# Optimization experiments

Hardware: AMD Instinct MI355X
Metric: run time of the kernel (lower is better)

The kernel has to match this reference:

```python
import jax, jax.numpy as jnp
import numpy as np
import math

RADIUS2 = 0.1 * 0.1   # QueryAndGroup(0.1, 64)
NSAMPLE = 64
NEG_SLOPE = 0.2


def get_lattice_points(b, n):
    # AtlasNet-style regular UV grid in [0,1]^2, first n points of a ceil(sqrt(n))^2 grid
    side = int(math.ceil(math.sqrt(n)))
    u = jnp.linspace(0.0, 1.0, side, dtype=jnp.float32)
    gx, gy = jnp.meshgrid(u, u, indexing='ij')
    pts = jnp.stack([gx.ravel(), gy.ravel()], axis=-1)[:n]  # (n, 2)
    return jnp.broadcast_to(pts[None], (b, n, 2))


def conv1x1(x, W, b):
    # 1x1 Conv1d == per-point GEMM: x (B,Cin,N), W (Cout,Cin), b (Cout,)
    return jnp.einsum('oc,bcn->bon', W, x) + b[None, :, None]


def mlp(x, params):
    for W, b in params:
        x = jax.nn.leaky_relu(conv1x1(x, W, b), NEG_SLOPE)
    return x


def ball_group_max(points, feats):
    # points (B,N,3), feats (B,C,N). Ball query (radius 0.1, first 64 in index
    # order, pad with first hit) + feature gather + max over neighborhood.
    B, N, _ = points.shape
    sq = jnp.sum(points * points, axis=-1)  # (B,N)
    d2 = sq[:, :, None] + sq[:, None, :] - 2.0 * jnp.einsum('bnd,bmd->bnm', points, points)
    mask = d2 < RADIUS2                                    # (B,N,N)
    cand = jnp.where(mask, jnp.arange(N, dtype=jnp.int32)[None, None, :], N)
    idx = jnp.sort(cand, axis=-1)[:, :, :NSAMPLE]          # first NSAMPLE hits
    first = idx[:, :, :1]
    idx = jnp.where(idx == N, first, idx)                  # pad with first hit (self always hits)
    idx = jnp.minimum(idx, N - 1)
    ft = jnp.swapaxes(feats, 1, 2)                         # (B,N,C)
    gathered = ft[jnp.arange(B)[:, None, None], idx]       # (B,N,K,C)
    return jnp.swapaxes(gathered.max(axis=2), 1, 2)        # (B,C,N)


def setup_inputs() -> dict:
    key = jax.random.key(0)
    ks = jax.random.split(key, 20)
    s = 0.05
    inp = {
        'z':   jax.random.normal(ks[0], (2, 512), dtype=jnp.float32),
        'W1a': jax.random.normal(ks[1], (512, 514), dtype=jnp.float32) * s,
        'b1a': jnp.zeros((512,), jnp.float32),
        'W1b': jax.random.normal(ks[2], (512, 512), dtype=jnp.float32) * s,
        'b1b': jnp.zeros((512,), jnp.float32),
        'W1c': jax.random.normal(ks[3], (512, 512), dtype=jnp.float32) * s,
        'b1c': jnp.zeros((512,), jnp.float32),
        'Wx1': jax.random.normal(ks[4], (3, 512), dtype=jnp.float32) * s,
        'bx1': jnp.zeros((3,), jnp.float32),
        'W2a': jax.random.normal(ks[5], (512, 1536), dtype=jnp.float32) * s,
        'b2a': jnp.zeros((512,), jnp.float32),
        'W2b': jax.random.normal(ks[6], (512, 512), dtype=jnp.float32) * s,
        'b2b': jnp.zeros((512,), jnp.float32),
        'W2c': jax.random.normal(ks[7], (512, 512), dtype=jnp.float32) * s,
        'b2c': jnp.zeros((512,), jnp.float32),
        'Wx2': jax.random.normal(ks[8], (3, 512), dtype=jnp.float32) * s,
        'bx2': jnp.zeros((3,), jnp.float32),
        'n1': 1024,
        'n2': 2048,
    }
    return inp


def reference(z, W1a, b1a, W1b, b1b, W1c, b1c, Wx1, bx1,
              W2a, b2a, W2b, b2b, W2c, b2c, Wx2, bx2, n1, n2):
    B, dim = z.shape

    def stage1(n):
        latt = get_lattice_points(B, n)                                    # (B,n,2)
        zc = jnp.concatenate([jnp.broadcast_to(z[:, None, :], (B, n, dim)), latt], axis=2)
        x = jnp.swapaxes(zc, 1, 2)                                         # (B,514,n)
        h = mlp(x, [(W1a, b1a), (W1b, b1b), (W1c, b1c)])                   # (B,512,n)
        pts = jnp.swapaxes(jax.nn.sigmoid(conv1x1(h, Wx1, bx1)), 1, 2) - 0.5
        return h, pts

    _, first_stage_points = stage1(n1)
    h2, fine_points = stage1(n2)

    local = ball_group_max(fine_points, h2)                                # (B,512,n2)
    glob = jnp.broadcast_to(h2.max(axis=2, keepdims=True), h2.shape)       # (B,512,n2)
    feat = jnp.concatenate([h2, local, glob], axis=1)                      # (B,1536,n2)

    f = mlp(feat, [(W2a, b2a), (W2b, b2b), (W2c, b2c)])
    delta = 0.1 * (jax.nn.sigmoid(conv1x1(f, Wx2, bx2)) - 0.5)
    second_stage_points = jnp.swapaxes(delta, 1, 2) + fine_points
    return (first_stage_points, second_stage_points, fine_points)
```

## Files before the change

kernel.cpp:

```cpp
#include <hip/hip_runtime.h>
#include <math.h>

#define B 2
#define N1 1024
#define N2 2048
#define R1TOT 6144
#define R2TOT 4096
#define SLOPE 0.2f

typedef short bf16x8 __attribute__((ext_vector_type(8)));
typedef float f32x4 __attribute__((ext_vector_type(4)));
typedef unsigned short u16x4 __attribute__((ext_vector_type(4)));
typedef unsigned short u16x8 __attribute__((ext_vector_type(8)));

__device__ __forceinline__ unsigned short f2bf(float x) {
    unsigned int u = __float_as_uint(x);
    unsigned int r = (u + 0x7fffu + ((u >> 16) & 1u)) >> 16;
    return (unsigned short)r;
}
__device__ __forceinline__ float bf2f(unsigned short h) {
    return __uint_as_float(((unsigned int)h) << 16);
}
__device__ __forceinline__ unsigned fenc(float f) {
    unsigned u = __float_as_uint(f);
    return (u & 0x80000000u) ? ~u : (u | 0x80000000u);
}
__device__ __forceinline__ float fdec(unsigned u) {
    unsigned b = (u & 0x80000000u) ? (u & 0x7FFFFFFFu) : ~u;
    return __uint_as_float(b);
}

#define OFF_WP     0
#define OFF_X1P    6291456
#define OFF_XMP    18874368
#define OFF_X2P    31457280
#define OFF_X3P    39845888
#define OFF_X4P    44040192
#define OFF_C1     48234496
#define OFF_GLOBE  48238592
#define OFF_GBIAS  48242688
#define OFF_HACC1  48246784
#define OFF_HACC2  48345088
#define ZERO_WORDS 43008

__global__ void k_prep(const float* __restrict__ W1b, const float* __restrict__ W1c,
                       const float* __restrict__ W2b, const float* __restrict__ W2c,
                       const float* __restrict__ W2a, unsigned short* __restrict__ wp,
                       const float* __restrict__ z, const float* __restrict__ W1a,
                       const float* __restrict__ b1a, float* __restrict__ c1,
                       float* __restrict__ zbase) {
    int bx = blockIdx.x, tid = threadIdx.x;
    if (bx < 6144) {
        int idx = bx * 256 + tid;
        const float* src; unsigned short* dst; int o, k, K, in_ld;
        if (idx < 1048576) {
            int which = idx >> 18; int local = idx & 262143;
            K = 512; in_ld = 512;
            src = (which == 0) ? W1b : (which == 1) ? W1c : (which == 2) ? W2b : W2c;
            dst = wp + (long)which * 524288;
            o = local >> 9; k = local & 511;
        } else {
            int local = idx - 1048576;
            K = 1024; in_ld = 1536; src = W2a; dst = wp + 2097152;
            o = local >> 10; k = local & 1023;
        }
        float v = src[(long)o * in_ld + k];
        unsigned short hi = f2bf(v);
        dst[(long)o * 2 * K + k] = hi;
        dst[(long)o * 2 * K + K + k] = f2bf(v - bf2f(hi));
    } else if (bx < 6152) {
        for (int l = (bx - 6144) * 256 + tid; l < ZERO_WORDS; l += 2048) zbase[l] = 0.f;
    } else {
        int gid = (bx - 6152) * 4 + (tid >> 6);
        int lane = tid & 63;
        int b = gid >> 9, o = gid & 511;
        float acc = 0.f;
        const float* wr = W1a + (long)o * 514;
        const float* zb = z + b * 512;
        for (int k = lane; k < 512; k += 64) acc += wr[k] * zb[k];
        #pragma unroll
        for (int off = 32; off > 0; off >>= 1) acc += __shfl_down(acc, off, 64);
        if (lane == 0) c1[gid] = acc + b1a[o];
    }
}

__global__ void k_layer_a(const float* __restrict__ W1a, const float* __restrict__ c1,
                          unsigned short* __restrict__ X1) {
    int idx = blockIdx.x * 256 + threadIdx.x;
    int o = idx & 511;
    int r = idx >> 9;
    int b, n, side;
    if (r < 2048) { b = r >> 10; n = r & 1023; side = 32; }
    else          { int r2 = r - 2048; b = r2 >> 11; n = r2 & 2047; side = 46; }
    int row = n / side, col = n % side;
    double inv = 1.0 / (double)(side - 1);
    float lx = (row == side - 1) ? 1.0f : (float)(row * inv);
    float ly = (col == side - 1) ? 1.0f : (float)(col * inv);
    float h = c1[b * 512 + o] + W1a[(long)o * 514 + 512] * lx + W1a[(long)o * 514 + 513] * ly;
    h = (h > 0.f) ? h : SLOPE * h;
    unsigned short hi = f2bf(h);
    X1[(long)r * 1024 + o] = hi;
    X1[(long)r * 1024 + 512 + o] = f2bf(h - bf2f(hi));
}

template<int TERMS>
__global__ __launch_bounds__(256, 2) void k_gemm(
    const unsigned short* __restrict__ Wp, int ldw,
    const unsigned short* __restrict__ Xp, int ldx,
    int K,
    const float* __restrict__ bias, int bias_div,
    unsigned short* __restrict__ Xn, int ldxn, int lo_off, int row_off, int pack_min,
    const float* __restrict__ Wx, float* __restrict__ hacc,
    unsigned* __restrict__ globE, int glob_min) {

    __shared__ __align__(16) char sm[32768];
    const int t = threadIdx.x;
    const int nb0 = blockIdx.x * 64;
    const int ob0 = blockIdx.y * 64;

    const unsigned short* gp[8];
    int lo_[8];
    #pragma unroll
    for (int p = 0; p < 8; ++p) {
        const int T = p >> 1;
        if (TERMS == 1 && (T == 1 || T == 3)) continue;
        int j2 = ((p & 1) << 8) + t;
        int r = j2 >> 3, cl = j2 & 7, cs = cl ^ (r & 7);
        gp[p] = (T < 2)
            ? (Wp + (long)(ob0 + r) * ldw + ((T == 1) ? K : 0) + cs * 8)
            : (Xp + (long)(nb0 + r) * ldx + ((T == 3) ? K : 0) + cs * 8);
        lo_[p] = p * 4096 + t * 16;
    }

    const int lane = t & 63, w = t >> 6;
    const int wy = w >> 1, wx = w & 1;
    const int quad = lane >> 4, l15 = lane & 15;
    const int xm = l15 & 7;
    const int rowA = (wy * 32 + l15) * 128;
    const int rowB = (wx * 32 + l15) * 128;
    const int ca0 = (quad ^ xm) * 16;
    const int ca1 = ((quad + 4) ^ xm) * 16;

    f32x4 acc[2][2];
    #pragma unroll
    for (int i = 0; i < 2; ++i)
        #pragma unroll
        for (int j = 0; j < 2; ++j) { f32x4 zz = {0.f, 0.f, 0.f, 0.f}; acc[i][j] = zz; }

    for (int k0 = 0; k0 < K; k0 += 64) {
        #pragma unroll
        for (int p = 0; p < 8; ++p) {
            const int T = p >> 1;
            if (TERMS == 1 && (T == 1 || T == 3)) continue;
            __builtin_amdgcn_global_load_lds(
                (const __attribute__((address_space(1))) void*)(const void*)(gp[p] + k0),
                (__attribute__((address_space(3))) void*)(void*)(sm + lo_[p]),
                16, 0, 0);
        }
        __syncthreads();
        #pragma unroll
        for (int sub = 0; sub < 2; ++sub) {
            const int cb = (sub == 0) ? ca0 : ca1;
            bf16x8 ah[2], bh[2];
            #pragma unroll
            for (int i = 0; i < 2; ++i)
                ah[i] = *(const bf16x8*)(const void*)(sm + rowA + i * 2048 + cb);
            #pragma unroll
            for (int j = 0; j < 2; ++j)
                bh[j] = *(const bf16x8*)(const void*)(sm + 16384 + rowB + j * 2048 + cb);
            if (TERMS == 3) {
                bf16x8 al[2], bl[2];
                #pragma unroll
                for (int i = 0; i < 2; ++i)
                    al[i] = *(const bf16x8*)(const void*)(sm + 8192 + rowA + i * 2048 + cb);
                #pragma unroll
                for (int j = 0; j < 2; ++j)
                    bl[j] = *(const bf16x8*)(const void*)(sm + 24576 + rowB + j * 2048 + cb);
                #pragma unroll
                for (int i = 0; i < 2; ++i)
                    #pragma unroll
                    for (int j = 0; j < 2; ++j) {
                        acc[i][j] = __builtin_amdgcn_mfma_f32_16x16x32_bf16(ah[i], bh[j], acc[i][j], 0, 0, 0);
                        acc[i][j] = __builtin_amdgcn_mfma_f32_16x16x32_bf16(ah[i], bl[j], acc[i][j], 0, 0, 0);
                        acc[i][j] = __builtin_amdgcn_mfma_f32_16x16x32_bf16(al[i], bh[j], acc[i][j], 0, 0, 0);
                    }
            } else {
                #pragma unroll
                for (int i = 0; i < 2; ++i)
                    #pragma unroll
                    for (int j = 0; j < 2; ++j)
                        acc[i][j] = __builtin_amdgcn_mfma_f32_16x16x32_bf16(ah[i], bh[j], acc[i][j], 0, 0, 0);
            }
        }
        __syncthreads();
    }

    float val[2][2][4];
    #pragma unroll
    for (int j = 0; j < 2; ++j) {
        int n = nb0 + wx * 32 + j * 16 + l15;
        int bidx0 = (bias_div >= (1 << 29)) ? 0 : (n / bias_div) * 512;
        #pragma unroll
        for (int i = 0; i < 2; ++i) {
            int ob = ob0 + wy * 32 + i * 16 + quad * 4;
            #pragma unroll
            for (int r = 0; r < 4; ++r) {
                float x = acc[i][j][r] + bias[bidx0 + ob + r];
                val[i][j][r] = (x > 0.f) ? x : SLOPE * x;
            }
        }
        if (Xn && n >= pack_min) {
            long nl = n - row_off;
            #pragma unroll
            for (int i = 0; i < 2; ++i) {
                int ob = ob0 + wy * 32 + i * 16 + quad * 4;
                u16x4 h4;
                #pragma unroll
                for (int r = 0; r < 4; ++r) h4[r] = f2bf(val[i][j][r]);
                *(u16x4*)(void*)(Xn + nl * ldxn + ob) = h4;
                if (lo_off) {
                    u16x4 l4;
                    #pragma unroll
                    for (int r = 0; r < 4; ++r) l4[r] = f2bf(val[i][j][r] - bf2f(h4[r]));
                    *(u16x4*)(void*)(Xn + nl * ldxn + lo_off + ob) = l4;
                }
            }
        }
    }

    if (hacc) {
        __syncthreads();
        float* smh = (float*)sm;
        unsigned* smg = (unsigned*)(sm + 1024);
        if (t < 256) smh[t] = 0.f;
        if (t < 64) smg[t] = 0u;
        __syncthreads();
        float wxv[3][2][4];
        #pragma unroll
        for (int ch = 0; ch < 3; ++ch)
            #pragma unroll
            for (int i = 0; i < 2; ++i)
                #pragma unroll
                for (int r = 0; r < 4; ++r)
                    wxv[ch][i][r] = Wx[ch * 512 + ob0 + wy * 32 + i * 16 + quad * 4 + r];
        #pragma unroll
        for (int j = 0; j < 2; ++j) {
            int nl = wx * 32 + j * 16 + l15;
            float p0 = 0.f, p1 = 0.f, p2 = 0.f;
            #pragma unroll
            for (int i = 0; i < 2; ++i)
                #pragma unroll
                for (int r = 0; r < 4; ++r) {
                    float v = val[i][j][r];
                    p0 += v * wxv[0][i][r];
                    p1 += v * wxv[1][i][r];
                    p2 += v * wxv[2][i][r];
                }
            atomicAdd(&smh[nl * 4 + 0], p0);
            atomicAdd(&smh[nl * 4 + 1], p1);
            atomicAdd(&smh[nl * 4 + 2], p2);
        }
        if (globE && nb0 >= glob_min) {
            #pragma unroll
            for (int i = 0; i < 2; ++i)
                #pragma unroll
                for (int r = 0; r < 4; ++r) {
                    float mx = fmaxf(val[i][0][r], val[i][1][r]);
                    atomicMax(&smg[wy * 32 + i * 16 + quad * 4 + r], fenc(mx));
                }
        }
        __syncthreads();
        if (t < 64) {
            atomicAdd(&hacc[(long)(nb0 + t) * 4 + 0], smh[t * 4 + 0]);
            atomicAdd(&hacc[(long)(nb0 + t) * 4 + 1], smh[t * 4 + 1]);
            atomicAdd(&hacc[(long)(nb0 + t) * 4 + 2], smh[t * 4 + 2]);
            if (globE && nb0 >= glob_min) {
                int b = (nb0 - glob_min) >> 11;
                atomicMax(&globE[b * 512 + ob0 + t], smg[t]);
            }
        }
    }
}

__global__ void k_finalize(const float* __restrict__ bx1, const float* __restrict__ hacc1,
                           float* __restrict__ out0, float* __restrict__ out2,
                           const float* __restrict__ W2a, const float* __restrict__ b2a,
                           const unsigned* __restrict__ globE, float* __restrict__ gbias) {
    int bx = blockIdx.x, tid = threadIdx.x;
    if (bx < 24) {
        int r = bx * 256 + tid;
        float* dst = (r < 2048) ? (out0 + (long)r * 3) : (out2 + (long)(r - 2048) * 3);
        #pragma unroll
        for (int ch = 0; ch < 3; ++ch) {
            float a = hacc1[(long)r * 4 + ch] + bx1[ch];
            dst[ch] = 1.f / (1.f + expf(-a)) - 0.5f;
        }
    } else {
        int gid = (bx - 24) * 4 + (tid >> 6);
        int lane = tid & 63;
        int b = gid >> 9, o = gid & 511;
        float acc = 0.f;
        const float* wr = W2a + (long)o * 1536 + 1024;
        for (int k = lane; k < 512; k += 64) acc += wr[k] * fdec(globE[b * 512 + k]);
        #pragma unroll
        for (int off = 32; off > 0; off >>= 1) acc += __shfl_down(acc, off, 64);
        if (lane == 0) gbias[gid] = acc + b2a[o];
    }
}

__global__ __launch_bounds__(256) void k_ball(const float* __restrict__ fine,
                                              unsigned short* __restrict__ X2P) {
    int i = blockIdx.x, b = blockIdx.y;
    int tid = threadIdx.x, lane = tid & 63, wv = tid >> 6;
    __shared__ int idxl[64];
    __shared__ int wcnt[4];
    __shared__ float part[8][256];
    const float* fb = fine + (long)b * N2 * 3;
    float xi = fb[i * 3 + 0], yi = fb[i * 3 + 1], zi = fb[i * 3 + 2];
    float sqi = __fadd_rn(__fadd_rn(__fmul_rn(xi, xi), __fmul_rn(yi, yi)), __fmul_rn(zi, zi));
    int cnt = 0;
    for (int it = 0; it < N2 / 256; ++it) {
        int j = it * 256 + tid;
        float xj = fb[j * 3 + 0], yj = fb[j * 3 + 1], zj = fb[j * 3 + 2];
        float sqj = __fadd_rn(__fadd_rn(__fmul_rn(xj, xj), __fmul_rn(yj, yj)), __fmul_rn(zj, zj));
        float dot = __fadd_rn(__fadd_rn(__fmul_rn(xi, xj), __fmul_rn(yi, yj)), __fmul_rn(zi, zj));
        float d2 = __fsub_rn(__fadd_rn(sqi, sqj), __fmul_rn(2.0f, dot));
        bool pred = d2 < 0.01f;
        unsigned long long m = __ballot(pred);
        if (lane == 0) wcnt[wv] = __popcll(m);
        __syncthreads();
        int wbase = cnt;
        #pragma unroll
        for (int q = 0; q < 3; ++q) { if (q < wv) wbase += wcnt[q]; }
        int total = wcnt[0] + wcnt[1] + wcnt[2] + wcnt[3];
        int rank = wbase + __popcll(m & ((1ull << lane) - 1ull));
        if (pred && rank < 64) idxl[rank] = j;
        cnt += total;
        if (cnt >= 64) break;
        __syncthreads();
    }
    __syncthreads();
    int m = min(cnt, 64);

    const unsigned short* hb = X2P + (long)b * N2 * 1024;
    int g = tid & 63, q = tid >> 6;
    float mx[8];
    #pragma unroll
    for (int r = 0; r < 8; ++r) mx[r] = -1e30f;
    for (int jj = q; jj < m; jj += 4) {
        u16x8 v = *(const u16x8*)(const void*)(hb + (long)idxl[jj] * 1024 + g * 8);
        #pragma unroll
        for (int r = 0; r < 8; ++r) mx[r] = fmaxf(mx[r], bf2f(v[r]));
    }
    #pragma unroll
    for (int r = 0; r < 8; ++r) part[r][tid] = mx[r];
    __syncthreads();
    if (tid < 64) {
        unsigned short* orow = X2P + (long)(b * N2 + i) * 1024;
        u16x8 hi;
        #pragma unroll
        for (int r = 0; r < 8; ++r) {
            float v0 = fmaxf(fmaxf(part[r][tid], part[r][tid + 64]),
                             fmaxf(part[r][tid + 128], part[r][tid + 192]));
            hi[r] = (unsigned short)(__float_as_uint(v0) >> 16);
        }
        *(u16x8*)(void*)(orow + 512 + tid * 8) = hi;
    }
}

__global__ void k_final2(const float* __restrict__ bx2, const float* __restrict__ hacc2,
                         const float* __restrict__ fine, float* __restrict__ out1) {
    int r = blockIdx.x * 256 + threadIdx.x;
    #pragma unroll
    for (int ch = 0; ch < 3; ++ch) {
        float a = hacc2[(long)r * 4 + ch] + bx2[ch];
        out1[(long)r * 3 + ch] = fine[(long)r * 3 + ch] + 0.1f * (1.f / (1.f + expf(-a)) - 0.5f);
    }
}

extern "C" void kernel_launch(void* const* d_in, const int* in_sizes, int n_in,
                              void* d_out, int out_size, void* d_ws, size_t ws_size,
                              hipStream_t stream) {
    const float* z   = (const float*)d_in[0];
    const float* W1a = (const float*)d_in[1];
    const float* b1a = (const float*)d_in[2];
    const float* W1b = (const float*)d_in[3];
    const float* b1b = (const float*)d_in[4];
    const float* W1c = (const float*)d_in[5];
    const float* b1c = (const float*)d_in[6];
    const float* Wx1 = (const float*)d_in[7];
    const float* bx1 = (const float*)d_in[8];
    const float* W2a = (const float*)d_in[9];
    const float* b2a = (const float*)d_in[10];
    const float* W2b = (const float*)d_in[11];
    const float* b2b = (const float*)d_in[12];
    const float* W2c = (const float*)d_in[13];
    const float* b2c = (const float*)d_in[14];
    const float* Wx2 = (const float*)d_in[15];
    const float* bx2 = (const float*)d_in[16];

    char* wsb = (char*)d_ws;
    unsigned short* WP   = (unsigned short*)(wsb + OFF_WP);
    unsigned short* X1P  = (unsigned short*)(wsb + OFF_X1P);
    unsigned short* XMP  = (unsigned short*)(wsb + OFF_XMP);
    unsigned short* X2P  = (unsigned short*)(wsb + OFF_X2P);
    unsigned short* X3P  = (unsigned short*)(wsb + OFF_X3P);
    unsigned short* X4P  = (unsigned short*)(wsb + OFF_X4P);
    float*    c1    = (float*)(wsb + OFF_C1);
    unsigned* globE = (unsigned*)(wsb + OFF_GLOBE);
    float*    gbias = (float*)(wsb + OFF_GBIAS);
    float*    hacc1 = (float*)(wsb + OFF_HACC1);
    float*    hacc2 = (float*)(wsb + OFF_HACC2);

    unsigned short* WP1b = WP;
    unsigned short* WP1c = WP + 524288;
    unsigned short* WP2b = WP + 1048576;
    unsigned short* WP2c = WP + 1572864;
    unsigned short* WP2a = WP + 2097152;

    float* out0 = (float*)d_out;
    float* out1 = out0 + B * N1 * 3;
    float* out2 = out1 + B * N2 * 3;
    float* fine = out2;

    const int BIG = 1 << 30;

    k_prep<<<6408, 256, 0, stream>>>(W1b, W1c, W2b, W2c, W2a, WP, z, W1a, b1a, c1,
                                     (float*)(wsb + OFF_GLOBE));
    k_layer_a<<<12288, 256, 0, stream>>>(W1a, c1, X1P);

    k_gemm<3><<<dim3(96, 8), 256, 0, stream>>>(WP1b, 1024, X1P, 1024, 512, b1b, BIG,
                                               XMP, 1024, 512, 0, 0,
                                               nullptr, nullptr, nullptr, 0);
    k_gemm<3><<<dim3(96, 8), 256, 0, stream>>>(WP1c, 1024, XMP, 1024, 512, b1c, BIG,
                                               X2P, 1024, 0, 2048, 2048,
                                               Wx1, hacc1, globE, 2048);
    k_finalize<<<280, 256, 0, stream>>>(bx1, hacc1, out0, out2, W2a, b2a, globE, gbias);
    k_ball<<<dim3(N2, B), 256, 0, stream>>>(fine, X2P);

    k_gemm<1><<<dim3(64, 8), 256, 0, stream>>>(WP2a, 2048, X2P, 1024, 1024, gbias, 2048,
                                               X3P, 512, 0, 0, 0,
                                               nullptr, nullptr, nullptr, 0);
    k_gemm<1><<<dim3(64, 8), 256, 0, stream>>>(WP2b, 1024, X3P, 512, 512, b2b, BIG,
                                               X4P, 512, 0, 0, 0,
                                               nullptr, nullptr, nullptr, 0);
    k_gemm<1><<<dim3(64, 8), 256, 0, stream>>>(WP2c, 1024, X4P, 512, 512, b2c, BIG,
                                               nullptr, 0, 0, 0, 0,
                                               Wx2, hacc2, nullptr, 0);
    k_final2<<<16, 256, 0, stream>>>(bx2, hacc2, fine, out1);
}
```

Baseline: 209.5 us.

## Double-buffer GEMM shared-memory tiles to overlap global loads with MFMA

Changes the GEMM main loop from load, sync, compute, sync to a two-buffer pipeline. The next K tile is issued via global_load_lds while MFMAs run on the current tile, with one barrier per iteration. The TERMS==1 variant also gets a compact 16KB-per-buffer layout so LDS doesn't grow for it. k_layer_a's block-to-row mapping and index math are tweaked to use shifts when the grid side is 32. Doubling LDS for the three-term variant may reduce occupancy.

```diff
diff --git a/kernel.cpp b/kernel.cpp
--- a/kernel.cpp
+++ b/kernel.cpp
@@ -86,13 +86,15 @@
 
 __global__ void k_layer_a(const float* __restrict__ W1a, const float* __restrict__ c1,
                           unsigned short* __restrict__ X1) {
-    int idx = blockIdx.x * 256 + threadIdx.x;
-    int o = idx & 511;
-    int r = idx >> 9;
+    int bx = blockIdx.x;
+    int r = bx >> 1;
+    int o = ((bx & 1) << 8) + threadIdx.x;
     int b, n, side;
     if (r < 2048) { b = r >> 10; n = r & 1023; side = 32; }
     else          { int r2 = r - 2048; b = r2 >> 11; n = r2 & 2047; side = 46; }
-    int row = n / side, col = n % side;
+    int row, col;
+    if (side == 32) { row = n >> 5; col = n & 31; }
+    else            { row = n / 46; col = n - row * 46; }
     double inv = 1.0 / (double)(side - 1);
     float lx = (row == side - 1) ? 1.0f : (float)(row * inv);
     float ly = (col == side - 1) ? 1.0f : (float)(col * inv);
@@ -113,7 +115,10 @@
     const float* __restrict__ Wx, float* __restrict__ hacc,
     unsigned* __restrict__ globE, int glob_min) {
 
-    __shared__ __align__(16) char sm[32768];
+    constexpr int BUFSZ = (TERMS == 3) ? 32768 : 16384;
+    constexpr int XBASE = (TERMS == 3) ? 16384 : 8192;
+    __shared__ __align__(16) char sm[2 * BUFSZ];
+
     const int t = threadIdx.x;
     const int nb0 = blockIdx.x * 64;
     const int ob0 = blockIdx.y * 64;
@@ -129,7 +134,8 @@
         gp[p] = (T < 2)
             ? (Wp + (long)(ob0 + r) * ldw + ((T == 1) ? K : 0) + cs * 8)
             : (Xp + (long)(nb0 + r) * ldx + ((T == 3) ? K : 0) + cs * 8);
-        lo_[p] = p * 4096 + t * 16;
+        const int reg = (TERMS == 3) ? p : ((p < 2) ? p : p - 2);
+        lo_[p] = reg * 4096 + t * 16;
     }
 
     const int lane = t & 63, w = t >> 6;
@@ -147,35 +153,38 @@
         #pragma unroll
         for (int j = 0; j < 2; ++j) { f32x4 zz = {0.f, 0.f, 0.f, 0.f}; acc[i][j] = zz; }
 
-    for (int k0 = 0; k0 < K; k0 += 64) {
+    auto stage = [&](int buf, int k0) {
         #pragma unroll
         for (int p = 0; p < 8; ++p) {
             const int T = p >> 1;
             if (TERMS == 1 && (T == 1 || T == 3)) continue;
             __builtin_amdgcn_global_load_lds(
                 (const __attribute__((address_space(1))) void*)(const void*)(gp[p] + k0),
-                (__attribute__((address_space(3))) void*)(void*)(sm + lo_[p]),
+                (__attribute__((address_space(3))) void*)(void*)(sm + buf * BUFSZ + lo_[p]),
                 16, 0, 0);
         }
-        __syncthreads();
+    };
+
+    auto compute = [&](int buf) {
+        char* smb = sm + buf * BUFSZ;
         #pragma unroll
         for (int sub = 0; sub < 2; ++sub) {
             const int cb = (sub == 0) ? ca0 : ca1;
             bf16x8 ah[2], bh[2];
             #pragma unroll
             for (int i = 0; i < 2; ++i)
-                ah[i] = *(const bf16x8*)(const void*)(sm + rowA + i * 2048 + cb);
+                ah[i] = *(const bf16x8*)(const void*)(smb + rowA + i * 2048 + cb);
             #pragma unroll
             for (int j = 0; j < 2; ++j)
-                bh[j] = *(const bf16x8*)(const void*)(sm + 16384 + rowB + j * 2048 + cb);
+                bh[j] = *(const bf16x8*)(const void*)(smb + XBASE + rowB + j * 2048 + cb);
             if (TERMS == 3) {
                 bf16x8 al[2], bl[2];
                 #pragma unroll
                 for (int i = 0; i < 2; ++i)
-                    al[i] = *(const bf16x8*)(const void*)(sm + 8192 + rowA + i * 2048 + cb);
+                    al[i] = *(const bf16x8*)(const void*)(smb + 8192 + rowA + i * 2048 + cb);
                 #pragma unroll
                 for (int j = 0; j < 2; ++j)
-                    bl[j] = *(const bf16x8*)(const void*)(sm + 24576 + rowB + j * 2048 + cb);
+                    bl[j] = *(const bf16x8*)(const void*)(smb + 24576 + rowB + j * 2048 + cb);
                 #pragma unroll
                 for (int i = 0; i < 2; ++i)
                     #pragma unroll
@@ -192,8 +201,18 @@
                         acc[i][j] = __builtin_amdgcn_mfma_f32_16x16x32_bf16(ah[i], bh[j], acc[i][j], 0, 0, 0);
             }
         }
-        __syncthreads();
-    }
+    };
+
+    stage(0, 0);
+    __syncthreads();
+    int cur = 0;
+    for (int k0 = 64; k0 < K; k0 += 64) {
+        stage(cur ^ 1, k0);
+        compute(cur);
+        __syncthreads();
+        cur ^= 1;
+    }
+    compute(cur);
 
     float val[2][2][4];
     #pragma unroll
```

Measured after the change: 211.8 us. About the same (+1.1%).

## Load GEMM operands straight from global into registers, dropping LDS staging

Applied to the files above, without the earlier changes.

The GEMM kernel no longer stages W and X tiles through a 32KB LDS buffer with global_load_lds and barriers. Each lane now loads its MFMA fragments directly from global memory, with K made a template parameter and the loop unrolled by two. LDS use shrinks to 1280 bytes and launch bounds rise to allow more resident blocks. k_layer_a also gets a block-to-row mapping and a shift/mask path for the 32-wide grid. The trade-off is redundant global and L2 traffic, since operand rows are re-read by every wave that needs them instead of being shared through LDS.

```diff
diff --git a/kernel.cpp b/kernel.cpp
--- a/kernel.cpp
+++ b/kernel.cpp
@@ -86,13 +86,15 @@
 
 __global__ void k_layer_a(const float* __restrict__ W1a, const float* __restrict__ c1,
                           unsigned short* __restrict__ X1) {
-    int idx = blockIdx.x * 256 + threadIdx.x;
-    int o = idx & 511;
-    int r = idx >> 9;
+    int bx = blockIdx.x;
+    int r = bx >> 1;
+    int o = ((bx & 1) << 8) + threadIdx.x;
     int b, n, side;
     if (r < 2048) { b = r >> 10; n = r & 1023; side = 32; }
     else          { int r2 = r - 2048; b = r2 >> 11; n = r2 & 2047; side = 46; }
-    int row = n / side, col = n % side;
+    int row, col;
+    if (side == 32) { row = n >> 5; col = n & 31; }
+    else            { row = n / 46; col = n - row * 46; }
     double inv = 1.0 / (double)(side - 1);
     float lx = (row == side - 1) ? 1.0f : (float)(row * inv);
     float ly = (col == side - 1) ? 1.0f : (float)(col * inv);
@@ -103,43 +105,30 @@
     X1[(long)r * 1024 + 512 + o] = f2bf(h - bf2f(hi));
 }
 
-template<int TERMS>
-__global__ __launch_bounds__(256, 2) void k_gemm(
+template<int TERMS, int KC>
+__global__ __launch_bounds__(256, (TERMS == 3) ? 3 : 4) void k_gemm(
     const unsigned short* __restrict__ Wp, int ldw,
     const unsigned short* __restrict__ Xp, int ldx,
-    int K,
     const float* __restrict__ bias, int bias_div,
     unsigned short* __restrict__ Xn, int ldxn, int lo_off, int row_off, int pack_min,
     const float* __restrict__ Wx, float* __restrict__ hacc,
     unsigned* __restrict__ globE, int glob_min) {
 
-    __shared__ __align__(16) char sm[32768];
+    __shared__ __align__(16) char sm[1280];
+
     const int t = threadIdx.x;
     const int nb0 = blockIdx.x * 64;
     const int ob0 = blockIdx.y * 64;
 
-    const unsigned short* gp[8];
-    int lo_[8];
-    #pragma unroll
-    for (int p = 0; p < 8; ++p) {
-        const int T = p >> 1;
-        if (TERMS == 1 && (T == 1 || T == 3)) continue;
-        int j2 = ((p & 1) << 8) + t;
-        int r = j2 >> 3, cl = j2 & 7, cs = cl ^ (r & 7);
-        gp[p] = (T < 2)
-            ? (Wp + (long)(ob0 + r) * ldw + ((T == 1) ? K : 0) + cs * 8)
-            : (Xp + (long)(nb0 + r) * ldx + ((T == 3) ? K : 0) + cs * 8);
-        lo_[p] = p * 4096 + t * 16;
-    }
-
     const int lane = t & 63, w = t >> 6;
     const int wy = w >> 1, wx = w & 1;
     const int quad = lane >> 4, l15 = lane & 15;
-    const int xm = l15 & 7;
-    const int rowA = (wy * 32 + l15) * 128;
-    const int rowB = (wx * 32 + l15) * 128;
-    const int ca0 = (quad ^ xm) * 16;
-    const int ca1 = ((quad + 4) ^ xm) * 16;
+    const int kb = quad * 8;
+
+    const unsigned short* a0 = Wp + (long)(ob0 + wy * 32 + 0  + l15) * ldw + kb;
+    const unsigned short* a1 = Wp + (long)(ob0 + wy * 32 + 16 + l15) * ldw + kb;
+    const unsigned short* b0 = Xp + (long)(nb0 + wx * 32 + 0  + l15) * ldx + kb;
+    const unsigned short* b1 = Xp + (long)(nb0 + wx * 32 + 16 + l15) * ldx + kb;
 
     f32x4 acc[2][2];
     #pragma unroll
@@ -147,52 +136,44 @@
         #pragma unroll
         for (int j = 0; j < 2; ++j) { f32x4 zz = {0.f, 0.f, 0.f, 0.f}; acc[i][j] = zz; }
 
-    for (int k0 = 0; k0 < K; k0 += 64) {
-        #pragma unroll
-        for (int p = 0; p < 8; ++p) {
-            const int T = p >> 1;
-            if (TERMS == 1 && (T == 1 || T == 3)) continue;
-            __builtin_amdgcn_global_load_lds(
-                (const __attribute__((address_space(1))) void*)(const void*)(gp[p] + k0),
-                (__attribute__((address_space(3))) void*)(void*)(sm + lo_[p]),
-                16, 0, 0);
-        }
-        __syncthreads();
-        #pragma unroll
-        for (int sub = 0; sub < 2; ++sub) {
-            const int cb = (sub == 0) ? ca0 : ca1;
-            bf16x8 ah[2], bh[2];
-            #pragma unroll
-            for (int i = 0; i < 2; ++i)
-                ah[i] = *(const bf16x8*)(const void*)(sm + rowA + i * 2048 + cb);
-            #pragma unroll
-            for (int j = 0; j < 2; ++j)
-                bh[j] = *(const bf16x8*)(const void*)(sm + 16384 + rowB + j * 2048 + cb);
-            if (TERMS == 3) {
-                bf16x8 al[2], bl[2];
-                #pragma unroll
-                for (int i = 0; i < 2; ++i)
-                    al[i] = *(const bf16x8*)(const void*)(sm + 8192 + rowA + i * 2048 + cb);
-                #pragma unroll
-                for (int j = 0; j < 2; ++j)
-                    bl[j] = *(const bf16x8*)(const void*)(sm + 24576 + rowB + j * 2048 + cb);
+    #pragma unroll 2
+    for (int k0 = 0; k0 < KC; k0 += 64) {
+        bf16x8 ah[2][2], bh[2][2];
+        #pragma unroll
+        for (int s = 0; s < 2; ++s) {
+            ah[0][s] = *(const bf16x8*)(const void*)(a0 + k0 + s * 32);
+            ah[1][s] = *(const bf16x8*)(const void*)(a1 + k0 + s * 32);
+            bh[0][s] = *(const bf16x8*)(const void*)(b0 + k0 + s * 32);
+            bh[1][s] = *(const bf16x8*)(const void*)(b1 + k0 + s * 32);
+        }
+        if constexpr (TERMS == 3) {
+            bf16x8 al[2][2], bl[2][2];
+            #pragma unroll
+            for (int s = 0; s < 2; ++s) {
+                al[0][s] = *(const bf16x8*)(const void*)(a0 + KC + k0 + s * 32);
+                al[1][s] = *(const bf16x8*)(const void*)(a1 + KC + k0 + s * 32);
+                bl[0][s] = *(const bf16x8*)(const void*)(b0 + KC + k0 + s * 32);
+                bl[1][s] = *(const bf16x8*)(const void*)(b1 + KC + k0 + s * 32);
+            }
+            #pragma unroll
+            for (int s = 0; s < 2; ++s)
                 #pragma unroll
                 for (int i = 0; i < 2; ++i)
                     #pragma unroll
                     for (int j = 0; j < 2; ++j) {
-                        acc[i][j] = __builtin_amdgcn_mfma_f32_16x16x32_bf16(ah[i], bh[j], acc[i][j], 0, 0, 0);
-                        acc[i][j] = __builtin_amdgcn_mfma_f32_16x16x32_bf16(ah[i], bl[j], acc[i][j], 0, 0, 0);
-                        acc[i][j] = __builtin_amdgcn_mfma_f32_16x16x32_bf16(al[i], bh[j], acc[i][j], 0, 0, 0);
+                        acc[i][j] = __builtin_amdgcn_mfma_f32_16x16x32_bf16(ah[i][s], bh[j][s], acc[i][j], 0, 0, 0);
+                        acc[i][j] = __builtin_amdgcn_mfma_f32_16x16x32_bf16(ah[i][s], bl[j][s], acc[i][j], 0, 0, 0);
+                        acc[i][j] = __builtin_amdgcn_mfma_f32_16x16x32_bf16(al[i][s], bh[j][s], acc[i][j], 0, 0, 0);
                     }
-            } else {
+        } else {
+            #pragma unroll
+            for (int s = 0; s < 2; ++s)
                 #pragma unroll
                 for (int i = 0; i < 2; ++i)
                     #pragma unroll
                     for (int j = 0; j < 2; ++j)
-                        acc[i][j] = __builtin_amdgcn_mfma_f32_16x16x32_bf16(ah[i], bh[j], acc[i][j], 0, 0, 0);
-            }
-        }
-        __syncthreads();
+                        acc[i][j] = __builtin_amdgcn_mfma_f32_16x16x32_bf16(ah[i][s], bh[j][s], acc[i][j], 0, 0, 0);
+        }
     }
 
     float val[2][2][4];
@@ -429,23 +410,23 @@
                                      (float*)(wsb + OFF_GLOBE));
     k_layer_a<<<12288, 256, 0, stream>>>(W1a, c1, X1P);
 
-    k_gemm<3><<<dim3(96, 8), 256, 0, stream>>>(WP1b, 1024, X1P, 1024, 512, b1b, BIG,
-                                               XMP, 1024, 512, 0, 0,
-                                               nullptr, nullptr, nullptr, 0);
-    k_gemm<3><<<dim3(96, 8), 256, 0, stream>>>(WP1c, 1024, XMP, 1024, 512, b1c, BIG,
-                                               X2P, 1024, 0, 2048, 2048,
-                                               Wx1, hacc1, globE, 2048);
+    k_gemm<3, 512><<<dim3(96, 8), 256, 0, stream>>>(WP1b, 1024, X1P, 1024, b1b, BIG,
+                                                    XMP, 1024, 512, 0, 0,
+                                                    nullptr, nullptr, nullptr, 0);
+    k_gemm<3, 512><<<dim3(96, 8), 256, 0, stream>>>(WP1c, 1024, XMP, 1024, b1c, BIG,
+                                                    X2P, 1024, 0, 2048, 2048,
+                                                    Wx1, hacc1, globE, 2048);
     k_finalize<<<280, 256, 0, stream>>>(bx1, hacc1, out0, out2, W2a, b2a, globE, gbias);
     k_ball<<<dim3(N2, B), 256, 0, stream>>>(fine, X2P);
 
-    k_gemm<1><<<dim3(64, 8), 256, 0, stream>>>(WP2a, 2048, X2P, 1024, 1024, gbias, 2048,
-                                               X3P, 512, 0, 0, 0,
-                                               nullptr, nullptr, nullptr, 0);
-    k_gemm<1><<<dim3(64, 8), 256, 0, stream>>>(WP2b, 1024, X3P, 512, 512, b2b, BIG,
-                                               X4P, 512, 0, 0, 0,
-                                               nullptr, nullptr, nullptr, 0);
-    k_gemm<1><<<dim3(64, 8), 256, 0, stream>>>(WP2c, 1024, X4P, 512, 512, b2c, BIG,
-                                               nullptr, 0, 0, 0, 0,
-                                               Wx2, hacc2, nullptr, 0);
+    k_gemm<1, 1024><<<dim3(64, 8), 256, 0, stream>>>(WP2a, 2048, X2P, 1024, gbias, 2048,
+                                                     X3P, 512, 0, 0, 0,
+                                                     nullptr, nullptr, nullptr, 0);
+    k_gemm<1, 512><<<dim3(64, 8), 256, 0, stream>>>(WP2b, 1024, X3P, 512, b2b, BIG,
+                                                    X4P, 512, 0, 0, 0,
+                                                    nullptr, nullptr, nullptr, 0);
+    k_gemm<1, 512><<<dim3(64, 8), 256, 0, stream>>>(WP2c, 1024, X4P, 512, b2c, BIG,
+                                                    nullptr, 0, 0, 0, 0,
+                                                    Wx2, hacc2, nullptr, 0);
     k_final2<<<16, 256, 0, stream>>>(bx2, hacc2, fine, out1);
 }
```

After: 306.6 us. 1.46x slower.
